# Kernel tuning notes

Hardware: AMD Instinct MI355X
Metric: run time of the kernel (lower is better)

Reference implementation:

```python
import jax, jax.numpy as jnp
import numpy as np

H = 64; W = 64; P = 16; NPH = 4; NPW = 4; PH = 16; PW = 16; ZD = 32; HD = 1024; UD = 3; B = 256


def affine_grid(theta, Ho, Wo):
    # torch F.affine_grid, align_corners=False. theta [N,2,3] -> grid [N,Ho,Wo,2]
    xs = (2.0 * jnp.arange(Wo, dtype=theta.dtype) + 1.0) / Wo - 1.0
    ys = (2.0 * jnp.arange(Ho, dtype=theta.dtype) + 1.0) / Ho - 1.0
    X, Y = jnp.meshgrid(xs, ys)  # [Ho,Wo] each, x varies along last axis
    base = jnp.stack([X, Y, jnp.ones_like(X)], axis=-1)  # [Ho,Wo,3]
    return jnp.einsum('nij,hwj->nhwi', theta, base)


def grid_sample(img, grid):
    # torch F.grid_sample bilinear, padding_mode='zeros', align_corners=False
    # img [N,H,W], grid [N,Ho,Wo,2] in [-1,1]
    Hi, Wi = img.shape[1], img.shape[2]
    x = (grid[..., 0] + 1.0) * Wi / 2.0 - 0.5
    y = (grid[..., 1] + 1.0) * Hi / 2.0 - 0.5
    x0 = jnp.floor(x); y0 = jnp.floor(y)
    wx = x - x0; wy = y - y0

    def gather(ix, iy):
        valid = (ix >= 0) & (ix < Wi) & (iy >= 0) & (iy < Hi)
        ixc = jnp.clip(ix, 0, Wi - 1).astype(jnp.int32)
        iyc = jnp.clip(iy, 0, Hi - 1).astype(jnp.int32)
        v = jax.vmap(lambda im, yy, xx: im[yy, xx])(img, iyc, ixc)
        return jnp.where(valid, v, 0.0)

    return (gather(x0, y0) * (1 - wx) * (1 - wy)
            + gather(x0 + 1, y0) * wx * (1 - wy)
            + gather(x0, y0 + 1) * (1 - wx) * wy
            + gather(x0 + 1, y0 + 1) * wx * wy)


def rot_tr(u):
    # rotTrMatrix: u [N,3] (angle, tx, ty) -> [N,2,3]
    c = jnp.cos(u[:, 0]); s = jnp.sin(u[:, 0])
    R = jnp.stack([jnp.stack([c, -s], -1), jnp.stack([s, c], -1)], -2)  # [N,2,2]
    return jnp.concatenate([R, u[:, 1:3, None]], axis=2)


def anchor_theta():
    # anchor_move: identity rotation + per-part grid-cell-center translations
    tx = (np.arange(NPW) * (W / NPW) + W / NPW / 2) / W - 0.5
    ty = (np.arange(NPH) * (H / NPH) + H / NPH / 2) / H - 0.5
    th = np.tile(np.concatenate([np.eye(2), np.zeros((2, 1))], axis=1)[None], (P, 1, 1)).astype(np.float32)
    for k in range(P):
        th[k, 0, 2] = tx[k % NPW]
        th[k, 1, 2] = ty[k // NPW]
    return jnp.asarray(th)


def forward(inputs, W1, b1, W2, b2, Wum, bum, Wuv, buv, Wgm, bgm, Wgv, bgv, Wz, M, eps_u, eps_g):
    hid = jax.nn.relu(inputs.reshape(-1, H * W) @ W1 + b1)
    hid = jax.nn.relu(hid @ W2 + b2)
    # global transform distribution (note: F.threshold(x,-6,6) -> 6 where x<=-6)
    gmu = jnp.tanh(hid @ Wgm + bgm)
    gpre = hid @ Wgv + bgv
    gvar = jnp.exp(jnp.where(gpre > -6.0, gpre, 6.0))
    gu = gmu + gvar * eps_g  # sample_u uses mu + var*eps (var, not std) as in source
    # per-part transform distribution (F.threshold(x,-6,-6) -> clamp below at -6)
    umu = jnp.tanh(hid @ Wum + bum)
    upre = hid @ Wuv + buv
    uvar = jnp.exp(jnp.where(upre > -6.0, upre, -6.0))
    u = (umu + uvar * eps_u).reshape(-1, UD)  # [B*P,3]
    # decode parts (input is ones, as in source)
    parts = jax.nn.sigmoid(jnp.ones((B, ZD), inputs.dtype) @ Wz).reshape(B * P, PH, PW)
    padh = (H - PH) // 2; padw = (W - PW) // 2
    parts = jnp.pad(parts, ((0, 0), (padh, H - PH - padh), (padw, W - PW - padw)))
    # anchor placement of parts and kernel masks
    th_a = jnp.tile(anchor_theta(), (B, 1, 1))  # [B*P,2,3], part-minor ordering
    g_a = affine_grid(th_a, H, W)
    parts = grid_sample(parts, g_a)                     # [B*P,H,W]
    KM = grid_sample(M[:B * P].reshape(B * P, H, W), g_a)
    # per-part rotation+translation for parts; translation-only for kernel
    theta = rot_tr(u)                                   # [B*P,2,3]
    g = affine_grid(theta, H, W)
    eye = jnp.broadcast_to(jnp.eye(2, dtype=theta.dtype), (B * P, 2, 2))
    theta_K = jnp.concatenate([eye, theta[:, :, 2:3]], axis=2)
    g_K = affine_grid(theta_K, H, W)
    KM = grid_sample(KM, g_K).reshape(B, P, H, W)
    xp = grid_sample(parts, g).reshape(B, P, H, W)
    # masked weighted compositing
    num = jnp.sum(xp * KM, axis=1)
    den = jnp.sum(KM, axis=1)
    den = jnp.where(den == 0.0, 1.0, den)
    x = num / den
    # global transform
    theta_g = rot_tr(gu)
    g_g = affine_grid(theta_g, H, W)
    return grid_sample(x, g_g)[:, None]  # [B,1,H,W]


def setup_inputs() -> dict:
    key = jax.random.key(0)
    ks = jax.random.split(key, 18)

    def lin(k, fin, fout):
        return jax.random.normal(k, (fin, fout), jnp.float32) / np.sqrt(fin)

    return {
        'inputs': jax.random.uniform(ks[0], (B, H * W), jnp.float32),
        'W1': lin(ks[1], H * W, HD), 'b1': jnp.zeros((HD,), jnp.float32),
        'W2': lin(ks[2], HD, HD), 'b2': jnp.zeros((HD,), jnp.float32),
        'Wum': lin(ks[3], HD, P * UD), 'bum': jnp.zeros((P * UD,), jnp.float32),
        'Wuv': lin(ks[4], HD, P * UD), 'buv': jnp.zeros((P * UD,), jnp.float32),
        'Wgm': lin(ks[5], HD, UD), 'bgm': jnp.zeros((UD,), jnp.float32),
        'Wgv': lin(ks[6], HD, UD), 'bgv': jnp.zeros((UD,), jnp.float32),
        'Wz': lin(ks[7], ZD, P * PH * PW),
        'M': jax.random.uniform(ks[8], (B * P, 1, H, W), jnp.float32),
        'eps_u': jax.random.normal(ks[9], (B, P * UD), jnp.float32),
        'eps_g': jax.random.normal(ks[10], (B, UD), jnp.float32),
    }


def reference(inputs, W1, b1, W2, b2, Wum, bum, Wuv, buv, Wgm, bgm, Wgv, bgv, Wz, M, eps_u, eps_g):
    return forward(inputs, W1, b1, W2, b2, Wum, bum, Wuv, buv, Wgm, bgm, Wgv, bgv, Wz, M, eps_u, eps_g)
```

## Files before the change

### kernel.cpp

```cpp
#include <hip/hip_runtime.h>
#include <math.h>

#define SPLITK 8

typedef __bf16 bf16x8 __attribute__((ext_vector_type(8)));
typedef float  f32x4  __attribute__((ext_vector_type(4)));

__device__ inline unsigned short bf16rne(float x) {
    unsigned int u = __float_as_uint(x);
    unsigned int r = u + 0x7FFFu + ((u >> 16) & 1u);
    return (unsigned short)(r >> 16);
}
__device__ inline float bf16tof(unsigned short h) {
    return __uint_as_float(((unsigned int)h) << 16);
}

__global__ __launch_bounds__(256) void prep_all(
    const float* __restrict__ inputs,
    const float* __restrict__ W1, const float* __restrict__ W2,
    const float* __restrict__ Wum, const float* __restrict__ Wuv,
    const float* __restrict__ Wgm, const float* __restrict__ Wgv,
    const float* __restrict__ Wz,
    unsigned short* __restrict__ Ahi, unsigned short* __restrict__ Alo,
    unsigned short* __restrict__ W1Thi, unsigned short* __restrict__ W1Tlo,
    unsigned short* __restrict__ W2Thi, unsigned short* __restrict__ W2Tlo,
    float* __restrict__ WT, float* __restrict__ partsb)
{
    __shared__ float t[32][33];
    int bid = blockIdx.x;
    int tid = threadIdx.x;
    if (bid < 4096 || (bid >= 5120 && bid < 6144)) {
        const float* W = (bid < 4096) ? W1 : W2;
        unsigned short* Thi = (bid < 4096) ? W1Thi : W2Thi;
        unsigned short* Tlo = (bid < 4096) ? W1Tlo : W2Tlo;
        int K = (bid < 4096) ? 4096 : 1024;
        int b2 = (bid < 4096) ? bid : (bid - 5120);
        int n0 = (b2 & 31) * 32, k0 = (b2 >> 5) * 32;
        int c = tid & 31, r0 = tid >> 5;
#pragma unroll
        for (int i = 0; i < 4; i++)
            t[r0 + 8 * i][c] = W[(size_t)(k0 + r0 + 8 * i) * 1024 + n0 + c];
        __syncthreads();
        int kk = tid & 31, n1 = tid >> 5;
#pragma unroll
        for (int i = 0; i < 4; i++) {
            float x = t[kk][n1 + 8 * i];
            unsigned short h = bf16rne(x);
            unsigned short l = bf16rne(x - bf16tof(h));
            size_t o = (size_t)(n0 + n1 + 8 * i) * K + k0 + kk;
            Thi[o] = h;
            Tlo[o] = l;
        }
    } else if (bid < 5120) {
        int id = ((bid - 4096) * 256 + tid) * 4;
        float4 x = *(const float4*)(inputs + id);
        ushort4 h, l;
        h.x = bf16rne(x.x); l.x = bf16rne(x.x - bf16tof(h.x));
        h.y = bf16rne(x.y); l.y = bf16rne(x.y - bf16tof(h.y));
        h.z = bf16rne(x.z); l.z = bf16rne(x.z - bf16tof(h.z));
        h.w = bf16rne(x.w); l.w = bf16rne(x.w - bf16tof(h.w));
        *(ushort4*)(Ahi + id) = h;
        *(ushort4*)(Alo + id) = l;
    } else if (bid < 6552) {
        int id = (bid - 6144) * 256 + tid;
        int o = id >> 10;
        int k = id & 1023;
        float v;
        if (o < 48)       v = Wum[k * 48 + o];
        else if (o < 96)  v = Wuv[k * 48 + (o - 48)];
        else if (o < 99)  v = Wgm[k * 3 + (o - 96)];
        else              v = Wgv[k * 3 + (o - 99)];
        WT[id] = v;
    } else {
        int idx = (bid - 6552) * 256 + tid;
        float s = 0.f;
#pragma unroll
        for (int z = 0; z < 32; z++) s += Wz[z * 4096 + idx];
        partsb[idx] = 1.f / (1.f + expf(-s));
    }
}

__global__ __launch_bounds__(256) void gemm_bf16x3(
    const unsigned short* __restrict__ Ahi, const unsigned short* __restrict__ Alo,
    const unsigned short* __restrict__ Bhi, const unsigned short* __restrict__ Blo,
    float* __restrict__ psum, int K, int kchunk)
{
    __shared__ unsigned short Ah[4096], Al[4096], Bh[4096], Bl[4096];
    int tid = threadIdx.x;
    int n0 = blockIdx.x * 64, m0 = blockIdx.y * 64;
    int kb = blockIdx.z * kchunk;
    int wid = tid >> 6, lane = tid & 63;
    int wm = wid & 1, wn = wid >> 1;
    int lm = lane & 15, q = lane >> 4;

    int r0 = tid >> 3, ch0 = tid & 7;
    int r1 = (tid + 256) >> 3, ch1 = (tid + 256) & 7;
    int l0 = r0 * 64 + 8 * (ch0 ^ (r0 & 7));
    int l1 = r1 * 64 + 8 * (ch1 ^ (r1 & 7));
    size_t ga0 = (size_t)(m0 + r0) * K + kb + ch0 * 8;
    size_t ga1 = (size_t)(m0 + r1) * K + kb + ch1 * 8;
    size_t gb0 = (size_t)(n0 + r0) * K + kb + ch0 * 8;
    size_t gb1 = (size_t)(n0 + r1) * K + kb + ch1 * 8;

    f32x4 acc[2][2] = {};

    int nkt = kchunk >> 6;
    uint4 vah0, vah1, val0, val1, vbh0, vbh1, vbl0, vbl1;
    vah0 = *(const uint4*)(Ahi + ga0);
    vah1 = *(const uint4*)(Ahi + ga1);
    val0 = *(const uint4*)(Alo + ga0);
    val1 = *(const uint4*)(Alo + ga1);
    vbh0 = *(const uint4*)(Bhi + gb0);
    vbh1 = *(const uint4*)(Bhi + gb1);
    vbl0 = *(const uint4*)(Blo + gb0);
    vbl1 = *(const uint4*)(Blo + gb1);

    int frm0 = (wm * 32 + lm) * 64;
    int frm1 = (wm * 32 + 16 + lm) * 64;
    int frn0 = (wn * 32 + lm) * 64;
    int frn1 = (wn * 32 + 16 + lm) * 64;
    int sw = lm & 7;

    for (int kt = 0; kt < nkt; kt++) {
        __syncthreads();
        *(uint4*)(Ah + l0) = vah0;
        *(uint4*)(Ah + l1) = vah1;
        *(uint4*)(Al + l0) = val0;
        *(uint4*)(Al + l1) = val1;
        *(uint4*)(Bh + l0) = vbh0;
        *(uint4*)(Bh + l1) = vbh1;
        *(uint4*)(Bl + l0) = vbl0;
        *(uint4*)(Bl + l1) = vbl1;
        __syncthreads();
        if (kt + 1 < nkt) {
            size_t o = (size_t)(kt + 1) * 64;
            vah0 = *(const uint4*)(Ahi + ga0 + o);
            vah1 = *(const uint4*)(Ahi + ga1 + o);
            val0 = *(const uint4*)(Alo + ga0 + o);
            val1 = *(const uint4*)(Alo + ga1 + o);
            vbh0 = *(const uint4*)(Bhi + gb0 + o);
            vbh1 = *(const uint4*)(Bhi + gb1 + o);
            vbl0 = *(const uint4*)(Blo + gb0 + o);
            vbl1 = *(const uint4*)(Blo + gb1 + o);
        }
#pragma unroll
        for (int ks = 0; ks < 2; ks++) {
            int cidx = 8 * (((ks << 2) + q) ^ sw);
            bf16x8 ah0 = *(const bf16x8*)(Ah + frm0 + cidx);
            bf16x8 ah1 = *(const bf16x8*)(Ah + frm1 + cidx);
            bf16x8 al0 = *(const bf16x8*)(Al + frm0 + cidx);
            bf16x8 al1 = *(const bf16x8*)(Al + frm1 + cidx);
            bf16x8 bh0 = *(const bf16x8*)(Bh + frn0 + cidx);
            bf16x8 bh1 = *(const bf16x8*)(Bh + frn1 + cidx);
            bf16x8 bl0 = *(const bf16x8*)(Bl + frn0 + cidx);
            bf16x8 bl1 = *(const bf16x8*)(Bl + frn1 + cidx);
            acc[0][0] = __builtin_amdgcn_mfma_f32_16x16x32_bf16(ah0, bh0, acc[0][0], 0, 0, 0);
            acc[0][0] = __builtin_amdgcn_mfma_f32_16x16x32_bf16(ah0, bl0, acc[0][0], 0, 0, 0);
            acc[0][0] = __builtin_amdgcn_mfma_f32_16x16x32_bf16(al0, bh0, acc[0][0], 0, 0, 0);
            acc[0][1] = __builtin_amdgcn_mfma_f32_16x16x32_bf16(ah0, bh1, acc[0][1], 0, 0, 0);
            acc[0][1] = __builtin_amdgcn_mfma_f32_16x16x32_bf16(ah0, bl1, acc[0][1], 0, 0, 0);
            acc[0][1] = __builtin_amdgcn_mfma_f32_16x16x32_bf16(al0, bh1, acc[0][1], 0, 0, 0);
            acc[1][0] = __builtin_amdgcn_mfma_f32_16x16x32_bf16(ah1, bh0, acc[1][0], 0, 0, 0);
            acc[1][0] = __builtin_amdgcn_mfma_f32_16x16x32_bf16(ah1, bl0, acc[1][0], 0, 0, 0);
            acc[1][0] = __builtin_amdgcn_mfma_f32_16x16x32_bf16(al1, bh0, acc[1][0], 0, 0, 0);
            acc[1][1] = __builtin_amdgcn_mfma_f32_16x16x32_bf16(ah1, bh1, acc[1][1], 0, 0, 0);
            acc[1][1] = __builtin_amdgcn_mfma_f32_16x16x32_bf16(ah1, bl1, acc[1][1], 0, 0, 0);
            acc[1][1] = __builtin_amdgcn_mfma_f32_16x16x32_bf16(al1, bh1, acc[1][1], 0, 0, 0);
        }
    }

    float* op = psum + (size_t)blockIdx.z * (256 * 1024);
#pragma unroll
    for (int mt = 0; mt < 2; mt++)
#pragma unroll
        for (int nt = 0; nt < 2; nt++) {
            int row = m0 + wm * 32 + mt * 16 + q * 4;
            int col = n0 + wn * 32 + nt * 16 + lm;
#pragma unroll
            for (int r = 0; r < 4; r++)
                op[(size_t)(row + r) * 1024 + col] = acc[mt][nt][r];
        }
}

__global__ __launch_bounds__(256) void reduce_bias_relu_split(
    const float* __restrict__ psum, const float* __restrict__ bias,
    unsigned short* __restrict__ hi, unsigned short* __restrict__ lo)
{
    int i = (blockIdx.x * 256 + threadIdx.x) * 4;
    float4 v = *(const float4*)(psum + i);
#pragma unroll
    for (int s = 1; s < SPLITK; s++) {
        float4 t = *(const float4*)(psum + (size_t)s * 262144 + i);
        v.x += t.x; v.y += t.y; v.z += t.z; v.w += t.w;
    }
    float4 bb = *(const float4*)(bias + (i & 1023));
    v.x = fmaxf(v.x + bb.x, 0.f);
    v.y = fmaxf(v.y + bb.y, 0.f);
    v.z = fmaxf(v.z + bb.z, 0.f);
    v.w = fmaxf(v.w + bb.w, 0.f);
    ushort4 h, l;
    h.x = bf16rne(v.x); l.x = bf16rne(v.x - bf16tof(h.x));
    h.y = bf16rne(v.y); l.y = bf16rne(v.y - bf16tof(h.y));
    h.z = bf16rne(v.z); l.z = bf16rne(v.z - bf16tof(h.z));
    h.w = bf16rne(v.w); l.w = bf16rne(v.w - bf16tof(h.w));
    *(ushort4*)(hi + i) = h;
    *(ushort4*)(lo + i) = l;
}

__global__ __launch_bounds__(512) void heads_v3(
    const float* __restrict__ psum, const float* __restrict__ b2,
    const float* __restrict__ WT,
    const float* __restrict__ bum, const float* __restrict__ buv,
    const float* __restrict__ bgm, const float* __restrict__ bgv,
    const float* __restrict__ eps_u, const float* __restrict__ eps_g,
    float* __restrict__ u_out, float* __restrict__ gu_out)
{
    int b = blockIdx.x;
    int tid = threadIdx.x;
    int w = tid >> 6, l = tid & 63;

    float4 hr[4];
#pragma unroll
    for (int i = 0; i < 4; i++) {
        int k = b * 1024 + i * 256 + l * 4;
        float4 acc = *(const float4*)(psum + k);
#pragma unroll
        for (int s = 1; s < SPLITK; s++) {
            float4 t = *(const float4*)(psum + (size_t)s * 262144 + k);
            acc.x += t.x; acc.y += t.y; acc.z += t.z; acc.w += t.w;
        }
        float4 bb = *(const float4*)(b2 + i * 256 + l * 4);
        acc.x = fmaxf(acc.x + bb.x, 0.f);
        acc.y = fmaxf(acc.y + bb.y, 0.f);
        acc.z = fmaxf(acc.z + bb.z, 0.f);
        acc.w = fmaxf(acc.w + bb.w, 0.f);
        hr[i] = acc;
    }

    int o = w;
    int rm = (o < 48) ? o : (48 + o);
    int rv = (o < 48) ? (o + 48) : (51 + o);
    float4 wm[4], wv[4];
    {
        const float* wp = WT + rm * 1024 + l * 4;
#pragma unroll
        for (int i = 0; i < 4; i++) wm[i] = *(const float4*)(wp + i * 256);
        wp = WT + rv * 1024 + l * 4;
#pragma unroll
        for (int i = 0; i < 4; i++) wv[i] = *(const float4*)(wp + i * 256);
    }

    while (o < 51) {
        int onext = o + 8;
        float4 wmn[4], wvn[4];
        if (onext < 51) {
            int rm2 = (onext < 48) ? onext : (48 + onext);
            int rv2 = (onext < 48) ? (onext + 48) : (51 + onext);
            const float* wp = WT + rm2 * 1024 + l * 4;
#pragma unroll
            for (int i = 0; i < 4; i++) wmn[i] = *(const float4*)(wp + i * 256);
            wp = WT + rv2 * 1024 + l * 4;
#pragma unroll
            for (int i = 0; i < 4; i++) wvn[i] = *(const float4*)(wp + i * 256);
        }
        float am = 0.f, av = 0.f;
#pragma unroll
        for (int i = 0; i < 4; i++) {
            am = fmaf(hr[i].x, wm[i].x, am);
            am = fmaf(hr[i].y, wm[i].y, am);
            am = fmaf(hr[i].z, wm[i].z, am);
            am = fmaf(hr[i].w, wm[i].w, am);
            av = fmaf(hr[i].x, wv[i].x, av);
            av = fmaf(hr[i].y, wv[i].y, av);
            av = fmaf(hr[i].z, wv[i].z, av);
            av = fmaf(hr[i].w, wv[i].w, av);
        }
#pragma unroll
        for (int s = 32; s; s >>= 1) {
            am += __shfl_xor(am, s, 64);
            av += __shfl_xor(av, s, 64);
        }
        if (l == 0) {
            if (o < 48) {
                float umu = tanhf(am + bum[o]);
                float uvar = expf(fmaxf(av + buv[o], -6.f));
                u_out[b * 48 + o] = umu + uvar * eps_u[b * 48 + o];
            } else {
                int n = o - 48;
                float gmu = tanhf(am + bgm[n]);
                float gpre = av + bgv[n];
                float gvar = expf(gpre > -6.f ? gpre : 6.f);
                gu_out[b * 3 + n] = gmu + gvar * eps_g[b * 3 + n];
            }
        }
#pragma unroll
        for (int i = 0; i < 4; i++) { wm[i] = wmn[i]; wv[i] = wvn[i]; }
        o = onext;
    }
}

__global__ __launch_bounds__(1024) void composite_final(
    const float* __restrict__ M, const float* __restrict__ parts,
    const float* __restrict__ u, const float* __restrict__ gu,
    float* __restrict__ out)
{
    __shared__ float patch[4096];
    __shared__ float plane[2][4096];
    __shared__ float pc[16], psn[16], ptx[16], pty[16];
    int b = blockIdx.x;
    int tid = threadIdx.x;

    for (int i = tid; i < 4096; i += 1024) patch[i] = parts[i];
    if (tid < 16) {
        const float* up = u + (b * 16 + tid) * 3;
        float ang = up[0];
        pc[tid] = cosf(ang);
        psn[tid] = sinf(ang);
        ptx[tid] = up[1];
        pty[tid] = up[2];
    }

    const float* Mb = M + ((size_t)(b * 16) << 12);
    ((float4*)plane[0])[tid] = ((const float4*)Mb)[tid];
    float4 pfn = ((const float4*)(Mb + 4096))[tid];
    __syncthreads();

    int j = tid & 63;
    int i0 = (tid >> 6) * 4;
    float xnv = (float)(2 * j + 1) * (1.f / 64.f) - 1.f;

    float num[4] = {}, den[4] = {};

    for (int p = 0; p < 16; p++) {
        int cur = p & 1;
        if (p + 1 < 16) ((float4*)plane[1 - cur])[tid] = pfn;
        if (p + 2 < 16) pfn = ((const float4*)(Mb + ((size_t)(p + 2) << 12)))[tid];

        int dx = 8 * (p & 3) - 12;
        int dy = 8 * (p >> 2) - 12;
        float c = pc[p], s = psn[p], tx = ptx[p], ty = pty[p];

        float ax = fminf(fmaxf(32.f * tx, -16384.f), 16384.f);
        float fax = floorf(ax);
        float wx = ax - fax;
        int ix = (int)fax;
        float ay = fminf(fmaxf(32.f * ty, -16384.f), 16384.f);
        float fay = floorf(ay);
        float wy = ay - fay;
        int iy = (int)fay;
        int iY = iy + dy;

        int x0 = j + ix;
        int X = x0 + dx;
        bool vc0 = ((unsigned)x0 < 64u) && ((unsigned)X < 64u);
        bool vc1 = ((unsigned)(x0 + 1) < 64u) && ((unsigned)(X + 1) < 64u);
        float w0 = vc0 ? (1.f - wx) : 0.f;
        float w1 = vc1 ? wx : 0.f;
        int Xc0 = min(max(X, 0), 63);
        int Xc1 = min(max(X + 1, 0), 63);

        const float* pl = plane[cur];
        float R[5];
#pragma unroll
        for (int r = 0; r < 5; r++) {
            int i = i0 + r;
            int ri = i + iY;
            bool vr = ((unsigned)(i + iy) < 64u) && ((unsigned)ri < 64u);
            int ric = min(max(ri, 0), 63);
            const float* row = pl + (ric << 6);
            float val = fmaf(w0, row[Xc0], w1 * row[Xc1]);
            R[r] = vr ? val : 0.f;
        }

        float Ax = fmaf(c, xnv, tx);
        float Ay = fmaf(s, xnv, ty);
        int ox = 24 - dx, oy = 24 - dy;
        float oxf = (float)ox, oyf = (float)oy;
        const float* pp = patch + (p << 8);
#pragma unroll
        for (int r = 0; r < 4; r++) {
            int i = i0 + r;
            float km = fmaf(wy, R[r + 1] - R[r], R[r]);
            den[r] += km;

            float ynv = (float)(2 * i + 1) * (1.f / 64.f) - 1.f;
            float gx = fmaf(-s, ynv, Ax);
            float gy = fmaf(c, ynv, Ay);
            float xs = fmaf(gx, 32.f, 31.5f);
            float ysv = fmaf(gy, 32.f, 31.5f);
            if (xs >= oxf - 1.f && xs < oxf + 16.f &&
                ysv >= oyf - 1.f && ysv < oyf + 16.f) {
                float xf = floorf(xs), yf = floorf(ysv);
                float wxx = xs - xf, wyy = ysv - yf;
                int a0 = (int)yf - oy;
                int b0c = (int)xf - ox;
                float v00 = 0.f, v10 = 0.f, v01 = 0.f, v11 = 0.f;
                if ((unsigned)a0 < 16u) {
                    const float* pr = pp + a0 * 16;
                    if ((unsigned)b0c < 16u) v00 = pr[b0c];
                    if ((unsigned)(b0c + 1) < 16u) v10 = pr[b0c + 1];
                }
                if ((unsigned)(a0 + 1) < 16u) {
                    const float* pr = pp + (a0 + 1) * 16;
                    if ((unsigned)b0c < 16u) v01 = pr[b0c];
                    if ((unsigned)(b0c + 1) < 16u) v11 = pr[b0c + 1];
                }
                float top = fmaf(wxx, v10 - v00, v00);
                float bot = fmaf(wxx, v11 - v01, v01);
                float xp = fmaf(wyy, bot - top, top);
                num[r] = fmaf(xp, km, num[r]);
            }
        }
        __syncthreads();
    }

    float* xl = plane[0];
#pragma unroll
    for (int r = 0; r < 4; r++) {
        float d = (den[r] == 0.f) ? 1.f : den[r];
        xl[(i0 + r) * 64 + j] = num[r] / d;
    }
    __syncthreads();

    float ang = gu[b * 3 + 0], gtx = gu[b * 3 + 1], gty = gu[b * 3 + 2];
    float cg = cosf(ang), sg = sinf(ang);
    float* ob = out + ((size_t)b << 12);
#pragma unroll
    for (int r = 0; r < 4; r++) {
        int i = i0 + r;
        float ynv = (float)(2 * i + 1) * (1.f / 64.f) - 1.f;
        float gx = cg * xnv - sg * ynv + gtx;
        float gy = sg * xnv + cg * ynv + gty;
        gx = fminf(fmaxf(gx, -8.f), 8.f);
        gy = fminf(fmaxf(gy, -8.f), 8.f);
        float xs = fmaf(gx, 32.f, 31.5f);
        float ysv = fmaf(gy, 32.f, 31.5f);
        float xf = floorf(xs), yf = floorf(ysv);
        float wx = xs - xf, wy = ysv - yf;
        int x0 = (int)xf, y0 = (int)yf;
        float v00 = 0.f, v10 = 0.f, v01 = 0.f, v11 = 0.f;
        bool vx0 = (unsigned)x0 < 64u, vx1 = (unsigned)(x0 + 1) < 64u;
        if ((unsigned)y0 < 64u) {
            const float* row = xl + y0 * 64;
            if (vx0) v00 = row[x0];
            if (vx1) v10 = row[x0 + 1];
        }
        if ((unsigned)(y0 + 1) < 64u) {
            const float* row = xl + (y0 + 1) * 64;
            if (vx0) v01 = row[x0];
            if (vx1) v11 = row[x0 + 1];
        }
        float top = fmaf(wx, v10 - v00, v00);
        float bot = fmaf(wx, v11 - v01, v01);
        ob[i * 64 + j] = fmaf(wy, bot - top, top);
    }
}

extern "C" void kernel_launch(void* const* d_in, const int* in_sizes, int n_in,
                              void* d_out, int out_size, void* d_ws, size_t ws_size,
                              hipStream_t stream)
{
    (void)in_sizes; (void)n_in; (void)out_size; (void)ws_size;
    const float* inputs = (const float*)d_in[0];
    const float* W1  = (const float*)d_in[1];
    const float* b1  = (const float*)d_in[2];
    const float* W2  = (const float*)d_in[3];
    const float* b2  = (const float*)d_in[4];
    const float* Wum = (const float*)d_in[5];
    const float* bum = (const float*)d_in[6];
    const float* Wuv = (const float*)d_in[7];
    const float* buv = (const float*)d_in[8];
    const float* Wgm = (const float*)d_in[9];
    const float* bgm = (const float*)d_in[10];
    const float* Wgv = (const float*)d_in[11];
    const float* bgv = (const float*)d_in[12];
    const float* Wz  = (const float*)d_in[13];
    const float* Mm  = (const float*)d_in[14];
    const float* eps_u = (const float*)d_in[15];
    const float* eps_g = (const float*)d_in[16];

    float* ws = (float*)d_ws;
    float* psum      = ws;
    float* u_buf     = ws + 2097152;
    float* gu_buf    = u_buf + 12288;
    float* parts_buf = gu_buf + 768;
    float* WTh_buf   = parts_buf + 4096;
    unsigned short* us = (unsigned short*)(WTh_buf + 104448);
    unsigned short* Ahi   = us;
    unsigned short* Alo   = Ahi + 1048576;
    unsigned short* W1Thi = Alo + 1048576;
    unsigned short* W1Tlo = W1Thi + 4194304;
    unsigned short* W2Thi = W1Tlo + 4194304;
    unsigned short* W2Tlo = W2Thi + 1048576;
    unsigned short* H1hi  = W2Tlo + 1048576;
    unsigned short* H1lo  = H1hi + 262144;

    prep_all<<<6568, 256, 0, stream>>>(inputs, W1, W2, Wum, Wuv, Wgm, Wgv, Wz,
                                       Ahi, Alo, W1Thi, W1Tlo, W2Thi, W2Tlo,
                                       WTh_buf, parts_buf);

    gemm_bf16x3<<<dim3(16, 4, SPLITK), 256, 0, stream>>>(Ahi, Alo, W1Thi, W1Tlo,
                                                         psum, 4096, 4096 / SPLITK);
    reduce_bias_relu_split<<<256, 256, 0, stream>>>(psum, b1, H1hi, H1lo);
    gemm_bf16x3<<<dim3(16, 4, SPLITK), 256, 0, stream>>>(H1hi, H1lo, W2Thi, W2Tlo,
                                                         psum, 1024, 1024 / SPLITK);
    heads_v3<<<256, 512, 0, stream>>>(psum, b2, WTh_buf, bum, buv, bgm, bgv,
                                      eps_u, eps_g, u_buf, gu_buf);
    composite_final<<<256, 1024, 0, stream>>>(Mm, parts_buf, u_buf, gu_buf,
                                              (float*)d_out);
}
```

Baseline: 199.2 us.

## Use 32x32x16 MFMA in split-bf16 GEMM and hoist per-part sampling setup

Each wave of the split-bf16 GEMM now computes its 32x32 tile with one 32x32x16 MFMA per term, in place of four 16x16x32 tiles. The hi*hi, hi*lo and lo*hi products go into three separate accumulators and are summed only at the end. This cuts LDS fragment loads and breaks the serial dependency chain between MFMAs. The composite kernel now computes the per-part floor/fraction translation terms once into shared memory and steps the sample coordinates incrementally across rows. Incremental stepping can change float rounding slightly near the bilinear bounds.

Result: no change. 198.0 us (-0.6%).

```diff
diff --git a/kernel.cpp b/kernel.cpp
--- a/kernel.cpp
+++ b/kernel.cpp
@@ -5,6 +5,7 @@
 
 typedef __bf16 bf16x8 __attribute__((ext_vector_type(8)));
 typedef float  f32x4  __attribute__((ext_vector_type(4)));
+typedef float  f32x16 __attribute__((ext_vector_type(16)));
 
 __device__ inline unsigned short bf16rne(float x) {
     unsigned int u = __float_as_uint(x);
@@ -91,7 +92,7 @@
     int kb = blockIdx.z * kchunk;
     int wid = tid >> 6, lane = tid & 63;
     int wm = wid & 1, wn = wid >> 1;
-    int lm = lane & 15, q = lane >> 4;
+    int lr = lane & 31, hi = lane >> 5;
 
     int r0 = tid >> 3, ch0 = tid & 7;
     int r1 = (tid + 256) >> 3, ch1 = (tid + 256) & 7;
@@ -102,7 +103,7 @@
     size_t gb0 = (size_t)(n0 + r0) * K + kb + ch0 * 8;
     size_t gb1 = (size_t)(n0 + r1) * K + kb + ch1 * 8;
 
-    f32x4 acc[2][2] = {};
+    f32x16 acc_hh = {}, acc_hl = {}, acc_lh = {};
 
     int nkt = kchunk >> 6;
     uint4 vah0, vah1, val0, val1, vbh0, vbh1, vbl0, vbl1;
@@ -115,11 +116,9 @@
     vbl0 = *(const uint4*)(Blo + gb0);
     vbl1 = *(const uint4*)(Blo + gb1);
 
-    int frm0 = (wm * 32 + lm) * 64;
-    int frm1 = (wm * 32 + 16 + lm) * 64;
-    int frn0 = (wn * 32 + lm) * 64;
-    int frn1 = (wn * 32 + 16 + lm) * 64;
-    int sw = lm & 7;
+    int basea = (wm * 32 + lr) * 64;
+    int baseb = (wn * 32 + lr) * 64;
+    int sw = lr & 7;
 
     for (int kt = 0; kt < nkt; kt++) {
         __syncthreads();
@@ -144,42 +143,26 @@
             vbl1 = *(const uint4*)(Blo + gb1 + o);
         }
 #pragma unroll
-        for (int ks = 0; ks < 2; ks++) {
-            int cidx = 8 * (((ks << 2) + q) ^ sw);
-            bf16x8 ah0 = *(const bf16x8*)(Ah + frm0 + cidx);
-            bf16x8 ah1 = *(const bf16x8*)(Ah + frm1 + cidx);
-            bf16x8 al0 = *(const bf16x8*)(Al + frm0 + cidx);
-            bf16x8 al1 = *(const bf16x8*)(Al + frm1 + cidx);
-            bf16x8 bh0 = *(const bf16x8*)(Bh + frn0 + cidx);
-            bf16x8 bh1 = *(const bf16x8*)(Bh + frn1 + cidx);
-            bf16x8 bl0 = *(const bf16x8*)(Bl + frn0 + cidx);
-            bf16x8 bl1 = *(const bf16x8*)(Bl + frn1 + cidx);
-            acc[0][0] = __builtin_amdgcn_mfma_f32_16x16x32_bf16(ah0, bh0, acc[0][0], 0, 0, 0);
-            acc[0][0] = __builtin_amdgcn_mfma_f32_16x16x32_bf16(ah0, bl0, acc[0][0], 0, 0, 0);
-            acc[0][0] = __builtin_amdgcn_mfma_f32_16x16x32_bf16(al0, bh0, acc[0][0], 0, 0, 0);
-            acc[0][1] = __builtin_amdgcn_mfma_f32_16x16x32_bf16(ah0, bh1, acc[0][1], 0, 0, 0);
-            acc[0][1] = __builtin_amdgcn_mfma_f32_16x16x32_bf16(ah0, bl1, acc[0][1], 0, 0, 0);
-            acc[0][1] = __builtin_amdgcn_mfma_f32_16x16x32_bf16(al0, bh1, acc[0][1], 0, 0, 0);
-            acc[1][0] = __builtin_amdgcn_mfma_f32_16x16x32_bf16(ah1, bh0, acc[1][0], 0, 0, 0);
-            acc[1][0] = __builtin_amdgcn_mfma_f32_16x16x32_bf16(ah1, bl0, acc[1][0], 0, 0, 0);
-            acc[1][0] = __builtin_amdgcn_mfma_f32_16x16x32_bf16(al1, bh0, acc[1][0], 0, 0, 0);
-            acc[1][1] = __builtin_amdgcn_mfma_f32_16x16x32_bf16(ah1, bh1, acc[1][1], 0, 0, 0);
-            acc[1][1] = __builtin_amdgcn_mfma_f32_16x16x32_bf16(ah1, bl1, acc[1][1], 0, 0, 0);
-            acc[1][1] = __builtin_amdgcn_mfma_f32_16x16x32_bf16(al1, bh1, acc[1][1], 0, 0, 0);
+        for (int s = 0; s < 4; s++) {
+            int cidx = 8 * (((s << 1) + hi) ^ sw);
+            bf16x8 afh = *(const bf16x8*)(Ah + basea + cidx);
+            bf16x8 afl = *(const bf16x8*)(Al + basea + cidx);
+            bf16x8 bfh = *(const bf16x8*)(Bh + baseb + cidx);
+            bf16x8 bfl = *(const bf16x8*)(Bl + baseb + cidx);
+            acc_hh = __builtin_amdgcn_mfma_f32_32x32x16_bf16(afh, bfh, acc_hh, 0, 0, 0);
+            acc_hl = __builtin_amdgcn_mfma_f32_32x32x16_bf16(afh, bfl, acc_hl, 0, 0, 0);
+            acc_lh = __builtin_amdgcn_mfma_f32_32x32x16_bf16(afl, bfh, acc_lh, 0, 0, 0);
         }
     }
 
     float* op = psum + (size_t)blockIdx.z * (256 * 1024);
-#pragma unroll
-    for (int mt = 0; mt < 2; mt++)
-#pragma unroll
-        for (int nt = 0; nt < 2; nt++) {
-            int row = m0 + wm * 32 + mt * 16 + q * 4;
-            int col = n0 + wn * 32 + nt * 16 + lm;
-#pragma unroll
-            for (int r = 0; r < 4; r++)
-                op[(size_t)(row + r) * 1024 + col] = acc[mt][nt][r];
-        }
+    int colg = n0 + wn * 32 + lr;
+#pragma unroll
+    for (int r = 0; r < 16; r++) {
+        int rowl = (r & 3) + 8 * (r >> 2) + 4 * hi;
+        float v = acc_hh[r] + acc_hl[r] + acc_lh[r];
+        op[(size_t)(m0 + wm * 32 + rowl) * 1024 + colg] = v;
+    }
 }
 
 __global__ __launch_bounds__(256) void reduce_bias_relu_split(
@@ -306,7 +289,8 @@
 {
     __shared__ float patch[4096];
     __shared__ float plane[2][4096];
-    __shared__ float pc[16], psn[16], ptx[16], pty[16];
+    __shared__ float pc[16], psn[16], ptx[16], pty[16], pwx[16], pwy[16];
+    __shared__ int pix[16], piy[16];
     int b = blockIdx.x;
     int tid = threadIdx.x;
 
@@ -316,8 +300,17 @@
         float ang = up[0];
         pc[tid] = cosf(ang);
         psn[tid] = sinf(ang);
-        ptx[tid] = up[1];
-        pty[tid] = up[2];
+        float tx = up[1], ty = up[2];
+        ptx[tid] = tx;
+        pty[tid] = ty;
+        float ax = fminf(fmaxf(32.f * tx, -16384.f), 16384.f);
+        float fax = floorf(ax);
+        pwx[tid] = ax - fax;
+        pix[tid] = (int)fax;
+        float ay = fminf(fmaxf(32.f * ty, -16384.f), 16384.f);
+        float fay = floorf(ay);
+        pwy[tid] = ay - fay;
+        piy[tid] = (int)fay;
     }
 
     const float* Mb = M + ((size_t)(b * 16) << 12);
@@ -328,6 +321,7 @@
     int j = tid & 63;
     int i0 = (tid >> 6) * 4;
     float xnv = (float)(2 * j + 1) * (1.f / 64.f) - 1.f;
+    float ynv0 = (float)(2 * i0 + 1) * (1.f / 64.f) - 1.f;
 
     float num[4] = {}, den[4] = {};
 
@@ -339,15 +333,8 @@
         int dx = 8 * (p & 3) - 12;
         int dy = 8 * (p >> 2) - 12;
         float c = pc[p], s = psn[p], tx = ptx[p], ty = pty[p];
-
-        float ax = fminf(fmaxf(32.f * tx, -16384.f), 16384.f);
-        float fax = floorf(ax);
-        float wx = ax - fax;
-        int ix = (int)fax;
-        float ay = fminf(fmaxf(32.f * ty, -16384.f), 16384.f);
-        float fay = floorf(ay);
-        float wy = ay - fay;
-        int iy = (int)fay;
+        float wx = pwx[p], wy = pwy[p];
+        int ix = pix[p], iy = piy[p];
         int iY = iy + dy;
 
         int x0 = j + ix;
@@ -372,22 +359,18 @@
             R[r] = vr ? val : 0.f;
         }
 
-        float Ax = fmaf(c, xnv, tx);
-        float Ay = fmaf(s, xnv, ty);
+        float gx0 = fmaf(-s, ynv0, fmaf(c, xnv, tx));
+        float gy0 = fmaf(c, ynv0, fmaf(s, xnv, ty));
+        float xs = fmaf(gx0, 32.f, 31.5f);
+        float ysv = fmaf(gy0, 32.f, 31.5f);
         int ox = 24 - dx, oy = 24 - dy;
         float oxf = (float)ox, oyf = (float)oy;
         const float* pp = patch + (p << 8);
 #pragma unroll
         for (int r = 0; r < 4; r++) {
-            int i = i0 + r;
             float km = fmaf(wy, R[r + 1] - R[r], R[r]);
             den[r] += km;
 
-            float ynv = (float)(2 * i + 1) * (1.f / 64.f) - 1.f;
-            float gx = fmaf(-s, ynv, Ax);
-            float gy = fmaf(c, ynv, Ay);
-            float xs = fmaf(gx, 32.f, 31.5f);
-            float ysv = fmaf(gy, 32.f, 31.5f);
             if (xs >= oxf - 1.f && xs < oxf + 16.f &&
                 ysv >= oyf - 1.f && ysv < oyf + 16.f) {
                 float xf = floorf(xs), yf = floorf(ysv);
@@ -410,6 +393,8 @@
                 float xp = fmaf(wyy, bot - top, top);
                 num[r] = fmaf(xp, km, num[r]);
             }
+            xs -= s;
+            ysv += c;
         }
         __syncthreads();
     }
```
